# Kernel optimization log

Hardware: AMD Instinct MI355X
Metric: run time of the kernel (lower is better)

Reference implementation:

```python
import jax, jax.numpy as jnp
import numpy as np

CORR_THRESHOLD = 0.5
EPS = 1e-12


def setup_inputs() -> dict:
    key = jax.random.key(0)
    # x: [B, N_channels, T] EEG windows
    x = jax.random.normal(key, (128, 64, 30720), dtype=jnp.float32)
    return {"x": x}


def reference(x):
    # Batched Pearson correlation across channels (rows = variables, like np.corrcoef).
    B, N, T = x.shape
    xc = x - jnp.mean(x, axis=-1, keepdims=True)            # center over time
    cov = jnp.einsum("bnt,bmt->bnm", xc, xc)                # [B, N, N] unnormalized
    norms = jnp.sqrt(jnp.einsum("bnt,bnt->bn", xc, xc))     # [B, N] row L2 norms
    corr = cov / (norms[:, :, None] * norms[:, None, :] + EPS)
    # zero diagonal, then threshold on |corr|
    eye = jnp.eye(N, dtype=bool)
    corr = jnp.where(eye[None], 0.0, corr)
    mask = jnp.abs(corr) >= CORR_THRESHOLD
    adj = jnp.where(mask, corr, 0.0)                        # dense masked adjacency [B, N, N]
    # node features are the raw EEG samples (as in the original Data(x=eeg_sample, ...))
    return adj, x
```

## Files before the change

kernel.cpp:

```cpp
#include <hip/hip_runtime.h>
#include <hip/hip_bf16.h>
#include <cstdint>
#include <cstddef>

#define B_   128
#define NCH  64
#define T_   30720
#define EPSF 1e-12f
#define THRF 0.5f

typedef float  f32x4 __attribute__((ext_vector_type(4)));
typedef short  s16x8 __attribute__((ext_vector_type(8)));
typedef unsigned short u16;

#define AS1 __attribute__((address_space(1)))
#define AS3 __attribute__((address_space(3)))

static __device__ __forceinline__ short bf16s(float f) {
    return (short)__builtin_bit_cast(u16, __float2bfloat16(f));
}

__global__ __launch_bounds__(256) void corr_stage1(
    const float* __restrict__ x, float* __restrict__ out_x,
    float* __restrict__ P, float* __restrict__ S,
    int split, int Tc)
{
    __shared__ __align__(16) float lds[2][NCH * 128];

    const int tid  = threadIdx.x;
    const int lane = tid & 63;
    const int w    = tid >> 6;

    const int bid = blockIdx.x;
    const int b   = bid / split;
    const int c   = bid - b * split;

    const size_t base = (size_t)b * ((size_t)NCH * T_) + (size_t)c * Tc;
    const float* xw = x + base;
    float*       ow = out_x + base;

    const int NT = Tc >> 7;

    const int sg = lane & 31;
    const int hi = lane >> 5;

    const int fr = lane & 15;
    const int g8 = lane >> 4;
    const int fs = fr & 7;

    f32x4 acc[4];
    #pragma unroll
    for (int cb = 0; cb < 4; ++cb) acc[cb] = (f32x4)(0.f);
    float csum[8];
    #pragma unroll
    for (int kk = 0; kk < 8; ++kk) csum[kk] = 0.f;

    auto dma = [&](int tile, int buf) {
        #pragma unroll
        for (int kk = 0; kk < 8; ++kk) {
            const int k  = w * 8 + kk;
            const int ch = 2 * k + hi;
            const int gg = sg ^ (ch & 7);
            const float* src = xw + (size_t)ch * T_ + (size_t)(tile * 128 + gg * 4);
            float* dst = &lds[buf][k * 256];
            __builtin_amdgcn_global_load_lds((const AS1 void*)src,
                                             (AS3 void*)dst, 16, 0, 0);
        }
    };

    dma(0, 0);
    asm volatile("s_waitcnt vmcnt(0)" ::: "memory");
    __builtin_amdgcn_s_barrier();
    __builtin_amdgcn_sched_barrier(0);

    for (int t = 0; t < NT; ++t) {
        const int cur = t & 1;
        if (t + 1 < NT) dma(t + 1, cur ^ 1);

        #pragma unroll
        for (int kk = 0; kk < 8; ++kk) {
            const int k   = w * 8 + kk;
            const int row = 2 * k + hi;
            const f32x4 v = *reinterpret_cast<const f32x4*>(
                &lds[cur][row * 128 + ((sg ^ (row & 7)) << 2)]);
            float* q = ow + (size_t)row * T_ + (size_t)(t * 128 + sg * 4);
            __builtin_nontemporal_store(v, reinterpret_cast<f32x4*>(q));
            csum[kk] += ((v.x + v.y) + (v.z + v.w));
        }

        #pragma unroll
        for (int ks = 0; ks < 4; ++ks) {
            const int g0 = ks * 8 + g8 * 2;
            const f32x4 alo = *reinterpret_cast<const f32x4*>(
                &lds[cur][(w * 16 + fr) * 128 + ((g0 ^ fs) << 2)]);
            const f32x4 ahi = *reinterpret_cast<const f32x4*>(
                &lds[cur][(w * 16 + fr) * 128 + (((g0 + 1) ^ fs) << 2)]);
            s16x8 Af;
            Af[0] = bf16s(alo.x); Af[1] = bf16s(alo.y);
            Af[2] = bf16s(alo.z); Af[3] = bf16s(alo.w);
            Af[4] = bf16s(ahi.x); Af[5] = bf16s(ahi.y);
            Af[6] = bf16s(ahi.z); Af[7] = bf16s(ahi.w);
            #pragma unroll
            for (int cb = 0; cb < 4; ++cb) {
                s16x8 Bf;
                if (cb == w) {
                    Bf = Af;
                } else {
                    const f32x4 blo = *reinterpret_cast<const f32x4*>(
                        &lds[cur][(cb * 16 + fr) * 128 + ((g0 ^ fs) << 2)]);
                    const f32x4 bhi = *reinterpret_cast<const f32x4*>(
                        &lds[cur][(cb * 16 + fr) * 128 + (((g0 + 1) ^ fs) << 2)]);
                    Bf[0] = bf16s(blo.x); Bf[1] = bf16s(blo.y);
                    Bf[2] = bf16s(blo.z); Bf[3] = bf16s(blo.w);
                    Bf[4] = bf16s(bhi.x); Bf[5] = bf16s(bhi.y);
                    Bf[6] = bf16s(bhi.z); Bf[7] = bf16s(bhi.w);
                }
                acc[cb] = __builtin_amdgcn_mfma_f32_16x16x32_bf16(Af, Bf, acc[cb], 0, 0, 0);
            }
        }

        asm volatile("s_waitcnt vmcnt(8)" ::: "memory");
        __builtin_amdgcn_s_barrier();
        __builtin_amdgcn_sched_barrier(0);
    }

    #pragma unroll
    for (int kk = 0; kk < 8; ++kk) {
        float v = csum[kk];
        v += __shfl_xor(v, 1,  64);
        v += __shfl_xor(v, 2,  64);
        v += __shfl_xor(v, 4,  64);
        v += __shfl_xor(v, 8,  64);
        v += __shfl_xor(v, 16, 64);
        if ((lane & 31) == 0) {
            const int row = 2 * (w * 8 + kk) + hi;
            S[(size_t)bid * NCH + row] = v;
        }
    }

    float* Pc = P + ((size_t)bid << 12);
    const int prow = (lane >> 4) << 2;
    const int pcol = lane & 15;
    #pragma unroll
    for (int cb = 0; cb < 4; ++cb)
        #pragma unroll
        for (int reg = 0; reg < 4; ++reg)
            Pc[(w * 16 + prow + reg) * 64 + cb * 16 + pcol] = acc[cb][reg];
}

__global__ __launch_bounds__(256) void corr_stage2(
    const float* __restrict__ P, const float* __restrict__ S,
    float* __restrict__ adj, int split)
{
    const int idx = blockIdx.x * 256 + threadIdx.x;
    const int b  = idx >> 12;
    const int nm = idx & 4095;
    const int n  = nm >> 6;
    const int m  = nm & 63;

    float G = 0.f, Gnn = 0.f, Gmm = 0.f, Sn = 0.f, Sm = 0.f;
    for (int c = 0; c < split; ++c) {
        const float* Pc = P + ((size_t)(b * split + c) << 12);
        const float* Sc = S + (size_t)(b * split + c) * NCH;
        G   += Pc[nm];
        Gnn += Pc[n * 65];
        Gmm += Pc[m * 65];
        Sn  += Sc[n];
        Sm  += Sc[m];
    }
    const float invT = 1.0f / (float)T_;
    const float cov  = G   - Sn * Sm * invT;
    const float vn   = Gnn - Sn * Sn * invT;
    const float vm   = Gmm - Sm * Sm * invT;
    const float den  = sqrtf(vn) * sqrtf(vm) + EPSF;
    float corr = cov / den;
    if (n == m) corr = 0.f;
    adj[idx] = (fabsf(corr) >= THRF) ? corr : 0.f;
}

extern "C" void kernel_launch(void* const* d_in, const int* in_sizes, int n_in,
                              void* d_out, int out_size, void* d_ws, size_t ws_size,
                              hipStream_t stream)
{
    const float* x   = (const float*)d_in[0];
    float* out   = (float*)d_out;
    float* adj   = out;
    float* out_x = out + (size_t)B_ * NCH * NCH;

    int split = 4;
    while (split > 1 &&
           (size_t)B_ * split * (4096 + NCH) * sizeof(float) > ws_size)
        split >>= 1;

    float* P = (float*)d_ws;
    float* S = P + (size_t)B_ * split * 4096;
    const int Tc = T_ / split;

    corr_stage1<<<dim3(B_ * split), dim3(256), 0, stream>>>(x, out_x, P, S, split, Tc);
    corr_stage2<<<dim3((B_ * 4096) / 256), dim3(256), 0, stream>>>(P, S, adj, split);
}
```

Measured before the change: 453.2 us.

## Give each wave its own time slice and full 64x64 Gram tile

After: 590.2 us. +30.2%, slower.

```diff
diff --git a/kernel.cpp b/kernel.cpp
--- a/kernel.cpp
+++ b/kernel.cpp
@@ -25,7 +25,7 @@
     float* __restrict__ P, float* __restrict__ S,
     int split, int Tc)
 {
-    __shared__ __align__(16) float lds[2][NCH * 128];
+    __shared__ __align__(16) float lds[4][2][NCH * 32];
 
     const int tid  = threadIdx.x;
     const int lane = tid & 63;
@@ -35,117 +35,113 @@
     const int b   = bid / split;
     const int c   = bid - b * split;
 
-    const size_t base = (size_t)b * ((size_t)NCH * T_) + (size_t)c * Tc;
+    const int tw0 = w * (Tc >> 2);
+    const size_t base = (size_t)b * ((size_t)NCH * T_) + (size_t)c * Tc + tw0;
     const float* xw = x + base;
     float*       ow = out_x + base;
 
-    const int NT = Tc >> 7;
-
-    const int sg = lane & 31;
-    const int hi = lane >> 5;
+    const int NK = Tc >> 7;
+
+    const int gsw = (lane & 7) ^ (lane >> 3);
+    const size_t srcBase = (size_t)(lane >> 3) * T_ + (size_t)(gsw * 4);
 
     const int fr = lane & 15;
     const int g8 = lane >> 4;
-    const int fs = fr & 7;
-
-    f32x4 acc[4];
-    #pragma unroll
-    for (int cb = 0; cb < 4; ++cb) acc[cb] = (f32x4)(0.f);
-    float csum[8];
-    #pragma unroll
-    for (int kk = 0; kk < 8; ++kk) csum[kk] = 0.f;
-
-    auto dma = [&](int tile, int buf) {
+    int offL[4], offH[4];
+    #pragma unroll
+    for (int rb = 0; rb < 4; ++rb) {
+        offL[rb] = rb * 512 + fr * 32 + (((2 * g8)     ^ (fr & 7)) << 2);
+        offH[rb] = rb * 512 + fr * 32 + (((2 * g8 + 1) ^ (fr & 7)) << 2);
+    }
+
+    f32x4 acc[4][4];
+    #pragma unroll
+    for (int rb = 0; rb < 4; ++rb)
+        #pragma unroll
+        for (int cb = 0; cb < 4; ++cb) acc[rb][cb] = (f32x4)(0.f);
+    float csum[4] = {0.f, 0.f, 0.f, 0.f};
+
+    auto dma = [&](int s, int buf) {
         #pragma unroll
         for (int kk = 0; kk < 8; ++kk) {
-            const int k  = w * 8 + kk;
-            const int ch = 2 * k + hi;
-            const int gg = sg ^ (ch & 7);
-            const float* src = xw + (size_t)ch * T_ + (size_t)(tile * 128 + gg * 4);
-            float* dst = &lds[buf][k * 256];
+            const float* src = xw + srcBase + (size_t)kk * (8 * T_) + (size_t)(s * 32);
+            float* dst = &lds[w][buf][kk * 256];
             __builtin_amdgcn_global_load_lds((const AS1 void*)src,
                                              (AS3 void*)dst, 16, 0, 0);
         }
     };
 
     dma(0, 0);
-    asm volatile("s_waitcnt vmcnt(0)" ::: "memory");
-    __builtin_amdgcn_s_barrier();
-    __builtin_amdgcn_sched_barrier(0);
-
-    for (int t = 0; t < NT; ++t) {
-        const int cur = t & 1;
-        if (t + 1 < NT) dma(t + 1, cur ^ 1);
-
-        #pragma unroll
-        for (int kk = 0; kk < 8; ++kk) {
-            const int k   = w * 8 + kk;
-            const int row = 2 * k + hi;
-            const f32x4 v = *reinterpret_cast<const f32x4*>(
-                &lds[cur][row * 128 + ((sg ^ (row & 7)) << 2)]);
-            float* q = ow + (size_t)row * T_ + (size_t)(t * 128 + sg * 4);
-            __builtin_nontemporal_store(v, reinterpret_cast<f32x4*>(q));
-            csum[kk] += ((v.x + v.y) + (v.z + v.w));
-        }
-
-        #pragma unroll
-        for (int ks = 0; ks < 4; ++ks) {
-            const int g0 = ks * 8 + g8 * 2;
-            const f32x4 alo = *reinterpret_cast<const f32x4*>(
-                &lds[cur][(w * 16 + fr) * 128 + ((g0 ^ fs) << 2)]);
-            const f32x4 ahi = *reinterpret_cast<const f32x4*>(
-                &lds[cur][(w * 16 + fr) * 128 + (((g0 + 1) ^ fs) << 2)]);
-            s16x8 Af;
-            Af[0] = bf16s(alo.x); Af[1] = bf16s(alo.y);
-            Af[2] = bf16s(alo.z); Af[3] = bf16s(alo.w);
-            Af[4] = bf16s(ahi.x); Af[5] = bf16s(ahi.y);
-            Af[6] = bf16s(ahi.z); Af[7] = bf16s(ahi.w);
+    dma(1, 1);
+
+    for (int s = 0; s < NK; ++s) {
+        if (s == 0 || s == NK - 1) {
+            asm volatile("s_waitcnt vmcnt(8)" ::: "memory");
+        } else {
+            asm volatile("s_waitcnt vmcnt(16)" ::: "memory");
+        }
+        __builtin_amdgcn_sched_barrier(0);
+
+        const float* Lw = lds[w][s & 1];
+        f32x4 lo[4], hi[4];
+        #pragma unroll
+        for (int rb = 0; rb < 4; ++rb) {
+            lo[rb] = *reinterpret_cast<const f32x4*>(&Lw[offL[rb]]);
+            hi[rb] = *reinterpret_cast<const f32x4*>(&Lw[offH[rb]]);
+        }
+
+        s16x8 A[4];
+        #pragma unroll
+        for (int rb = 0; rb < 4; ++rb) {
+            float* q = ow + (size_t)(rb * 16 + fr) * T_ + (size_t)(s * 32 + g8 * 8);
+            __builtin_nontemporal_store(lo[rb], reinterpret_cast<f32x4*>(q));
+            __builtin_nontemporal_store(hi[rb], reinterpret_cast<f32x4*>(q + 4));
+            csum[rb] += ((lo[rb].x + lo[rb].y) + (lo[rb].z + lo[rb].w))
+                      + ((hi[rb].x + hi[rb].y) + (hi[rb].z + hi[rb].w));
+            A[rb][0] = bf16s(lo[rb].x); A[rb][1] = bf16s(lo[rb].y);
+            A[rb][2] = bf16s(lo[rb].z); A[rb][3] = bf16s(lo[rb].w);
+            A[rb][4] = bf16s(hi[rb].x); A[rb][5] = bf16s(hi[rb].y);
+            A[rb][6] = bf16s(hi[rb].z); A[rb][7] = bf16s(hi[rb].w);
+        }
+
+        #pragma unroll
+        for (int rb = 0; rb < 4; ++rb)
             #pragma unroll
-            for (int cb = 0; cb < 4; ++cb) {
-                s16x8 Bf;
-                if (cb == w) {
-                    Bf = Af;
-                } else {
-                    const f32x4 blo = *reinterpret_cast<const f32x4*>(
-                        &lds[cur][(cb * 16 + fr) * 128 + ((g0 ^ fs) << 2)]);
-                    const f32x4 bhi = *reinterpret_cast<const f32x4*>(
-                        &lds[cur][(cb * 16 + fr) * 128 + (((g0 + 1) ^ fs) << 2)]);
-                    Bf[0] = bf16s(blo.x); Bf[1] = bf16s(blo.y);
-                    Bf[2] = bf16s(blo.z); Bf[3] = bf16s(blo.w);
-                    Bf[4] = bf16s(bhi.x); Bf[5] = bf16s(bhi.y);
-                    Bf[6] = bf16s(bhi.z); Bf[7] = bf16s(bhi.w);
-                }
-                acc[cb] = __builtin_amdgcn_mfma_f32_16x16x32_bf16(Af, Bf, acc[cb], 0, 0, 0);
-            }
-        }
-
-        asm volatile("s_waitcnt vmcnt(8)" ::: "memory");
-        __builtin_amdgcn_s_barrier();
-        __builtin_amdgcn_sched_barrier(0);
-    }
-
-    #pragma unroll
-    for (int kk = 0; kk < 8; ++kk) {
-        float v = csum[kk];
-        v += __shfl_xor(v, 1,  64);
-        v += __shfl_xor(v, 2,  64);
-        v += __shfl_xor(v, 4,  64);
-        v += __shfl_xor(v, 8,  64);
+            for (int cb = 0; cb < 4; ++cb)
+                acc[rb][cb] = __builtin_amdgcn_mfma_f32_16x16x32_bf16(
+                    A[rb], A[cb], acc[rb][cb], 0, 0, 0);
+
+        if (s + 2 < NK) {
+            __builtin_amdgcn_sched_barrier(0);
+            dma(s + 2, s & 1);
+        }
+    }
+
+    #pragma unroll
+    for (int rb = 0; rb < 4; ++rb) {
+        float v = csum[rb];
         v += __shfl_xor(v, 16, 64);
-        if ((lane & 31) == 0) {
-            const int row = 2 * (w * 8 + kk) + hi;
-            S[(size_t)bid * NCH + row] = v;
-        }
-    }
-
-    float* Pc = P + ((size_t)bid << 12);
+        v += __shfl_xor(v, 32, 64);
+        if (lane < 16)
+            S[((size_t)bid * 4 + w) * 64 + rb * 16 + lane] = v;
+    }
+
+    float* st = &lds[0][0][0];
     const int prow = (lane >> 4) << 2;
     const int pcol = lane & 15;
     #pragma unroll
-    for (int cb = 0; cb < 4; ++cb)
-        #pragma unroll
-        for (int reg = 0; reg < 4; ++reg)
-            Pc[(w * 16 + prow + reg) * 64 + cb * 16 + pcol] = acc[cb][reg];
+    for (int rb = 0; rb < 4; ++rb)
+        #pragma unroll
+        for (int cb = 0; cb < 4; ++cb)
+            #pragma unroll
+            for (int reg = 0; reg < 4; ++reg)
+                st[w * 4096 + (rb * 16 + prow + reg) * 64 + cb * 16 + pcol]
+                    = acc[rb][cb][reg];
+    __syncthreads();
+
+    float* Pc = P + ((size_t)bid << 12);
+    for (int i = tid; i < 4096; i += 256)
+        Pc[i] = (st[i] + st[4096 + i]) + (st[8192 + i] + st[12288 + i]);
 }
 
 __global__ __launch_bounds__(256) void corr_stage2(
@@ -160,13 +156,17 @@
 
     float G = 0.f, Gnn = 0.f, Gmm = 0.f, Sn = 0.f, Sm = 0.f;
     for (int c = 0; c < split; ++c) {
-        const float* Pc = P + ((size_t)(b * split + c) << 12);
-        const float* Sc = S + (size_t)(b * split + c) * NCH;
+        const int bc = b * split + c;
+        const float* Pc = P + ((size_t)bc << 12);
         G   += Pc[nm];
         Gnn += Pc[n * 65];
         Gmm += Pc[m * 65];
-        Sn  += Sc[n];
-        Sm  += Sc[m];
+        #pragma unroll
+        for (int w = 0; w < 4; ++w) {
+            const float* Sc = S + ((size_t)bc * 4 + w) * 64;
+            Sn += Sc[n];
+            Sm += Sc[m];
+        }
     }
     const float invT = 1.0f / (float)T_;
     const float cov  = G   - Sn * Sm * invT;
@@ -189,7 +189,7 @@
 
     int split = 4;
     while (split > 1 &&
-           (size_t)B_ * split * (4096 + NCH) * sizeof(float) > ws_size)
+           (size_t)B_ * split * (4096 + 4 * 64) * sizeof(float) > ws_size)
         split >>= 1;
 
     float* P = (float*)d_ws;
```
